# Kernel tuning notes

Hardware: AMD Instinct MI355X
Metric: run time of the kernel (lower is better)

Reference implementation:

```python
import jax, jax.numpy as jnp
import numpy as np

MARGIN = 0.25


def _cdist(x, y):
    # Euclidean distance matrix, same math as torch.cdist(p=2).
    # x: [M, D], y: [K, D] -> [M, K]
    sq = (
        jnp.sum(x * x, axis=1, keepdims=True)
        + jnp.sum(y * y, axis=1)[None, :]
        - 2.0 * (x @ y.T)
    )
    return jnp.sqrt(jnp.maximum(sq, 0.0))


def setup_inputs() -> dict:
    key = jax.random.key(0)
    k1, k2, k3 = jax.random.split(key, 3)
    B, P, N, D = 2048, 2048, 16, 128
    anchor = jax.random.normal(k1, (B, D), dtype=jnp.float32)
    positive = jax.random.normal(k2, (P, D), dtype=jnp.float32)
    negative = jax.random.normal(k3, (B, N, D), dtype=jnp.float32)
    return {"anchor": anchor, "positive": positive, "negative": negative}


def reference(anchor, positive, negative):
    B, N, D = negative.shape
    # hardest positive: max distance to any positive, per anchor -> [B]
    d_pos = _cdist(anchor, positive).max(axis=1)
    # Original torch code expands negatives across a redundant batch dim and
    # takes min over the flattened (B*B*N); per row this equals the GLOBAL min
    # over all anchor-negative pairs. Compute it without the duplication.
    neg_flat = negative.reshape(B * N, D)  # [B*N, D]
    d_neg = _cdist(anchor, neg_flat).min()  # scalar
    losses = jax.nn.relu(d_pos - d_neg + MARGIN)  # [B]
    return losses.mean()
```

## Files before the change

kernel.cpp:

```cpp
#include <hip/hip_runtime.h>
#include <hip/hip_bf16.h>

#define MARGIN_F 0.25f

#define B_ANCH 2048
#define P_POS  2048
#define N_NEG  32768
#define DDIM   128

#define QS    (6.0f / 127.0f)
#define QINV  (127.0f / 6.0f)
#define QC    (2.0f * QS * QS)
#define QCI   (1.0f / QC)

typedef __attribute__((ext_vector_type(4))) float f32x4;
typedef __attribute__((ext_vector_type(4))) int   i32x4;

__device__ __forceinline__ int q8(float x, float scl) {
    int q = __float2int_rn(x * scl);
    return max(-127, min(127, q));
}

__global__ __launch_bounds__(256) void prep_kernel(
    const float* __restrict__ anchor, const float* __restrict__ positive,
    const float* __restrict__ negative,
    signed char* __restrict__ qA, signed char* __restrict__ qP,
    signed char* __restrict__ qN,
    float* __restrict__ nA, int* __restrict__ npI, int* __restrict__ nnI,
    unsigned* __restrict__ dposBits, unsigned* __restrict__ dnegBits,
    unsigned* __restrict__ doneCnt)
{
    const int tile = blockIdx.x * 4 + (threadIdx.x >> 6);
    const int lane = threadIdx.x & 63;
    const int lm = lane & 15, lk = lane >> 4;

    if (blockIdx.x == 0 && threadIdx.x == 0) {
        *dnegBits = 0x7F800000u;
        *doneCnt  = 0u;
    }

    const float* src; signed char* dst; int t; float scl; int kind;
    if (tile < 128)      { src = anchor;   dst = qA; t = tile;       scl = -QINV; kind = 0; }
    else if (tile < 256) { src = positive; dst = qP; t = tile - 128; scl =  QINV; kind = 1; }
    else                 { src = negative; dst = qN; t = tile - 256; scl =  QINV; kind = 2; }

    if (kind == 0 && lm == lane) dposBits[t * 16 + lm] = 0u;

    const int row = t * 16 + lm;
    float ss = 0.f;
    #pragma unroll
    for (int s = 0; s < 2; ++s) {
        const float* sp = src + (size_t)row * DDIM + s * 64 + lk * 16;
        float v[16];
        #pragma unroll
        for (int c4 = 0; c4 < 4; ++c4) {
            float4 vv = *(const float4*)(sp + c4 * 4);
            v[c4*4+0]=vv.x; v[c4*4+1]=vv.y; v[c4*4+2]=vv.z; v[c4*4+3]=vv.w;
        }
        #pragma unroll
        for (int j = 0; j < 16; ++j) ss += v[j] * v[j];
        i32x4 o;
        #pragma unroll
        for (int w = 0; w < 4; ++w) {
            int b0 = q8(v[w*4+0], scl) & 255;
            int b1 = q8(v[w*4+1], scl) & 255;
            int b2 = q8(v[w*4+2], scl) & 255;
            int b3 = q8(v[w*4+3], scl) & 255;
            o[w] = b0 | (b1 << 8) | (b2 << 16) | (b3 << 24);
        }
        *(i32x4*)(dst + ((size_t)(t * 2 + s) * 64 + lane) * 16) = o;
    }
    ss += __shfl_xor(ss, 16);
    ss += __shfl_xor(ss, 32);
    if (lk == 0) {
        if (kind == 0)      nA[row]  = ss;
        else if (kind == 1) npI[row] = __float2int_rn(ss * QCI);
        else                nnI[row] = __float2int_rn(ss * QCI);
    }
}

template<int MODE, int CT>
__device__ __forceinline__ void i8_tile(
    const i32x4* __restrict__ Aq, const i32x4* __restrict__ Yq,
    const float* __restrict__ nAf, const int* __restrict__ nyI,
    int by, int bx,
    unsigned* __restrict__ dposBits, unsigned* __restrict__ dnegBits)
{
    const int wid  = threadIdx.x >> 6;
    const int lane = threadIdx.x & 63;
    const int lm = lane & 15, lk = lane >> 4;
    const int wr = wid >> 1, wc = wid & 1;
    const int rt0 = by * 8 + wr * 4;

    i32x4 a[4][2];
    #pragma unroll
    for (int m = 0; m < 4; ++m)
        #pragma unroll
        for (int s = 0; s < 2; ++s)
            a[m][s] = Aq[(size_t)((rt0 + m) * 2 + s) * 64 + lane];

    int redI[4][4];
    #pragma unroll
    for (int m = 0; m < 4; ++m)
        #pragma unroll
        for (int r = 0; r < 4; ++r)
            redI[m][r] = (MODE == 0) ? (int)0x80000000 : 0x7FFFFFFF;

    constexpr int G = CT * 4;
    auto ctile_of = [&](int p) {
        return (bx * CT + (p >> 2)) * 8 + wc * 4 + (p & 3);
    };

    i32x4 b[3][2];
    int nyv[3];
    #pragma unroll
    for (int p = 0; p < 2 && p < G; ++p) {
        const int ctile = ctile_of(p);
        #pragma unroll
        for (int s = 0; s < 2; ++s)
            b[p][s] = Yq[(size_t)(ctile * 2 + s) * 64 + lane];
        nyv[p] = nyI[ctile * 16 + lm];
    }

    #pragma unroll
    for (int g = 0; g < G; ++g) {
        const int cb = g % 3;
        if (g + 2 < G) {
            const int ctile = ctile_of(g + 2);
            #pragma unroll
            for (int s = 0; s < 2; ++s)
                b[(g + 2) % 3][s] = Yq[(size_t)(ctile * 2 + s) * 64 + lane];
            nyv[(g + 2) % 3] = nyI[ctile * 16 + lm];
        }
        const int ny = nyv[cb];
        const i32x4 cvec = {ny, ny, ny, ny};
        i32x4 acc[4];
        #pragma unroll
        for (int m = 0; m < 4; ++m)
            acc[m] = __builtin_amdgcn_mfma_i32_16x16x64_i8(a[m][0], b[cb][0], cvec, 0, 0, 0);
        #pragma unroll
        for (int m = 0; m < 4; ++m)
            acc[m] = __builtin_amdgcn_mfma_i32_16x16x64_i8(a[m][1], b[cb][1], acc[m], 0, 0, 0);
        #pragma unroll
        for (int m = 0; m < 4; ++m)
            #pragma unroll
            for (int r = 0; r < 4; ++r)
                redI[m][r] = (MODE == 0) ? max(redI[m][r], acc[m][r])
                                         : min(redI[m][r], acc[m][r]);
    }

    if (MODE == 0) {
        #pragma unroll
        for (int msk = 1; msk < 16; msk <<= 1)
            #pragma unroll
            for (int m = 0; m < 4; ++m)
                #pragma unroll
                for (int r = 0; r < 4; ++r)
                    redI[m][r] = max(redI[m][r], __shfl_xor(redI[m][r], msk));
        if (lm == 0) {
            #pragma unroll
            for (int m = 0; m < 4; ++m)
                #pragma unroll
                for (int r = 0; r < 4; ++r) {
                    const int row = (rt0 + m) * 16 + 4 * lk + r;
                    const float sq =
                        fmaxf(__builtin_fmaf(QC, (float)redI[m][r], nAf[row]), 0.f);
                    atomicMax(dposBits + row, __float_as_uint(sq));
                }
        }
    } else {
        float mn = 3.4e38f;
        #pragma unroll
        for (int m = 0; m < 4; ++m)
            #pragma unroll
            for (int r = 0; r < 4; ++r) {
                const float na = nAf[(rt0 + m) * 16 + 4 * lk + r];
                mn = fminf(mn, __builtin_fmaf(QC, (float)redI[m][r], na));
            }
        mn = fmaxf(mn, 0.f);
        #pragma unroll
        for (int msk = 1; msk < 64; msk <<= 1) mn = fminf(mn, __shfl_xor(mn, msk));
        __shared__ float wmin[4];
        if (lane == 0) wmin[wid] = mn;
        __syncthreads();
        if (threadIdx.x == 0) {
            const float m2 = fminf(fminf(wmin[0], wmin[1]), fminf(wmin[2], wmin[3]));
            atomicMin(dnegBits, __float_as_uint(m2));
        }
    }
}

#define POS_BLOCKS 256
#define NEG_BLOCKS 512
#define TOT_BLOCKS (POS_BLOCKS + NEG_BLOCKS)

__global__ __launch_bounds__(256, 3) void fused_dist_kernel(
    const signed char* __restrict__ qA, const signed char* __restrict__ qP,
    const signed char* __restrict__ qN,
    const float* __restrict__ nA, const int* __restrict__ npI,
    const int* __restrict__ nnI,
    unsigned* __restrict__ dposBits, unsigned* __restrict__ dnegBits,
    unsigned* __restrict__ doneCnt, float* __restrict__ out)
{
    const int bid = blockIdx.x;
    if (bid < POS_BLOCKS) {
        i8_tile<0, 1>((const i32x4*)qA, (const i32x4*)qP, nA, npI,
                      bid >> 4, bid & 15, dposBits, dnegBits);
    } else {
        const int q = bid - POS_BLOCKS;
        i8_tile<1, 8>((const i32x4*)qA, (const i32x4*)qN, nA, nnI,
                      q >> 5, q & 31, dposBits, dnegBits);
    }

    asm volatile("s_waitcnt vmcnt(0)" ::: "memory");
    __syncthreads();
    __shared__ unsigned lastFlag;
    if (threadIdx.x == 0)
        lastFlag = (atomicAdd(doneCnt, 1u) == TOT_BLOCKS - 1) ? 1u : 0u;
    __syncthreads();
    if (lastFlag) {
        const float dneg = sqrtf(__uint_as_float(atomicAdd(dnegBits, 0u)));
        float s = 0.f;
        for (int i = threadIdx.x; i < B_ANCH; i += 256) {
            const float dp = sqrtf(__uint_as_float(atomicAdd(dposBits + i, 0u)));
            s += fmaxf(dp - dneg + MARGIN_F, 0.f);
        }
        #pragma unroll
        for (int m = 1; m < 64; m <<= 1) s += __shfl_xor(s, m);
        __shared__ float ws4[4];
        const int wid = threadIdx.x >> 6, lane = threadIdx.x & 63;
        if (lane == 0) ws4[wid] = s;
        __syncthreads();
        if (threadIdx.x == 0)
            out[0] = (ws4[0] + ws4[1] + ws4[2] + ws4[3]) * (1.f / (float)B_ANCH);
    }
}

extern "C" void kernel_launch(void* const* d_in, const int* in_sizes, int n_in,
                              void* d_out, int out_size, void* d_ws, size_t ws_size,
                              hipStream_t stream) {
    const float* anchor   = (const float*)d_in[0];
    const float* positive = (const float*)d_in[1];
    const float* negative = (const float*)d_in[2];
    float* out = (float*)d_out;

    char* ws = (char*)d_ws;
    size_t off = 0;
    auto alloc = [&](size_t bytes) { char* p = ws + off; off = (off + bytes + 255) & ~(size_t)255; return p; };

    signed char* qA = (signed char*)alloc((size_t)B_ANCH * DDIM);
    signed char* qP = (signed char*)alloc((size_t)P_POS  * DDIM);
    signed char* qN = (signed char*)alloc((size_t)N_NEG  * DDIM);
    float* nA  = (float*)alloc((size_t)B_ANCH * 4);
    int*   npI = (int*)alloc((size_t)P_POS  * 4);
    int*   nnI = (int*)alloc((size_t)N_NEG  * 4);
    unsigned* dposBits = (unsigned*)alloc((size_t)B_ANCH * 4);
    unsigned* dnegBits = (unsigned*)alloc(4);
    unsigned* doneCnt  = (unsigned*)alloc(4);

    prep_kernel<<<576, 256, 0, stream>>>(
        anchor, positive, negative, qA, qP, qN, nA, npI, nnI,
        dposBits, dnegBits, doneCnt);

    fused_dist_kernel<<<TOT_BLOCKS, 256, 0, stream>>>(
        qA, qP, qN, nA, npI, nnI, dposBits, dnegBits, doneCnt, out);
}
```

Before: 30.89 us.

## Stage negative tiles in LDS via double-buffered direct global-to-LDS loads

The negative-distance path now copies each 8-column-tile chunk of quantized negatives into shared memory with global_load_lds, double-buffered across 8 chunks, so both wave columns share one fetch instead of loading B fragments straight into registers. The positive path is split into its own simpler function without the rotating register prefetch. This aims to cut redundant global traffic and register pressure in the dominant negative blocks. In exchange it allocates 32 KB of LDS per block, which can limit occupancy for all blocks including the positive ones, and adds a barrier per chunk.

```diff
diff --git a/kernel.cpp b/kernel.cpp
--- a/kernel.cpp
+++ b/kernel.cpp
@@ -79,12 +79,125 @@
     }
 }
 
-template<int MODE, int CT>
-__device__ __forceinline__ void i8_tile(
+__device__ __forceinline__ i32x4 mfma_i8(i32x4 a, i32x4 b, i32x4 c) {
+    return __builtin_amdgcn_mfma_i32_16x16x64_i8(a, b, c, 0, 0, 0);
+}
+
+__device__ __forceinline__ void gload_lds16(const void* g, void* l) {
+    typedef const __attribute__((address_space(1))) unsigned int as1_u32;
+    typedef __attribute__((address_space(3))) unsigned int as3_u32;
+    __builtin_amdgcn_global_load_lds(
+        (as1_u32*)(reinterpret_cast<uintptr_t>(g)),
+        (as3_u32*)(reinterpret_cast<uintptr_t>(l)),
+        16, 0, 0);
+}
+
+#define LDS_TILE 16384
+
+__device__ __forceinline__ void neg_tile_lds(
+    const i32x4* __restrict__ Aq, const signed char* __restrict__ qN,
+    const float* __restrict__ nAf, const int* __restrict__ nyI,
+    int by, int bx, unsigned* __restrict__ dnegBits,
+    signed char* __restrict__ ldsB)
+{
+    const int tid  = threadIdx.x;
+    const int wid  = tid >> 6;
+    const int lane = tid & 63;
+    const int lm = lane & 15, lk = lane >> 4;
+    const int wr = wid >> 1, wc = wid & 1;
+    const int rt0 = by * 8 + wr * 4;
+
+    i32x4 a[4][2];
+    #pragma unroll
+    for (int m = 0; m < 4; ++m)
+        #pragma unroll
+        for (int s = 0; s < 2; ++s)
+            a[m][s] = Aq[(size_t)((rt0 + m) * 2 + s) * 64 + lane];
+
+    int redI[4][4];
+    #pragma unroll
+    for (int m = 0; m < 4; ++m)
+        #pragma unroll
+        for (int r = 0; r < 4; ++r) redI[m][r] = 0x7FFFFFFF;
+
+    {
+        const signed char* g = qN + (size_t)(bx * 64) * 2048;
+        signed char* lw = ldsB + wid * 1024;
+        #pragma unroll
+        for (int c = 0; c < 4; ++c)
+            gload_lds16(g + c * 4096 + tid * 16, lw + c * 4096);
+    }
+    asm volatile("s_waitcnt vmcnt(0)" ::: "memory");
+    __syncthreads();
+
+    #pragma unroll 1
+    for (int ct = 0; ct < 8; ++ct) {
+        const signed char* lb = ldsB + (ct & 1) * LDS_TILE;
+        if (ct + 1 < 8) {
+            const signed char* g = qN + (size_t)(bx * 64 + (ct + 1) * 8) * 2048;
+            signed char* lw = ldsB + ((ct & 1) ^ 1) * LDS_TILE + wid * 1024;
+            #pragma unroll
+            for (int c = 0; c < 4; ++c)
+                gload_lds16(g + c * 4096 + tid * 16, lw + c * 4096);
+        }
+        const int ctb = (bx * 64 + ct * 8 + wc * 4) * 16 + lm;
+        const int ny0 = nyI[ctb +  0];
+        const int ny1 = nyI[ctb + 16];
+        const int ny2 = nyI[ctb + 32];
+        const int ny3 = nyI[ctb + 48];
+
+        #pragma unroll
+        for (int g4 = 0; g4 < 4; ++g4) {
+            const signed char* bp = lb + (size_t)((wc * 4 + g4) * 2) * 1024 + lane * 16;
+            const i32x4 b0 = *(const i32x4*)(bp);
+            const i32x4 b1 = *(const i32x4*)(bp + 1024);
+            const int nyc = (g4 == 0) ? ny0 : (g4 == 1) ? ny1 : (g4 == 2) ? ny2 : ny3;
+            const i32x4 cvec = {nyc, nyc, nyc, nyc};
+            i32x4 c0 = mfma_i8(a[0][0], b0, cvec);
+            i32x4 c1 = mfma_i8(a[1][0], b0, cvec);
+            i32x4 c2 = mfma_i8(a[2][0], b0, cvec);
+            i32x4 c3 = mfma_i8(a[3][0], b0, cvec);
+            c0 = mfma_i8(a[0][1], b1, c0);
+            c1 = mfma_i8(a[1][1], b1, c1);
+            c2 = mfma_i8(a[2][1], b1, c2);
+            c3 = mfma_i8(a[3][1], b1, c3);
+            #pragma unroll
+            for (int rr = 0; rr < 4; ++rr) {
+                redI[0][rr] = min(redI[0][rr], c0[rr]);
+                redI[1][rr] = min(redI[1][rr], c1[rr]);
+                redI[2][rr] = min(redI[2][rr], c2[rr]);
+                redI[3][rr] = min(redI[3][rr], c3[rr]);
+            }
+        }
+
+        asm volatile("s_waitcnt vmcnt(0)" ::: "memory");
+        __syncthreads();
+    }
+
+    float mn = 3.4e38f;
+    #pragma unroll
+    for (int m = 0; m < 4; ++m)
+        #pragma unroll
+        for (int r = 0; r < 4; ++r) {
+            const float na = nAf[(rt0 + m) * 16 + 4 * lk + r];
+            mn = fminf(mn, __builtin_fmaf(QC, (float)redI[m][r], na));
+        }
+    mn = fmaxf(mn, 0.f);
+    #pragma unroll
+    for (int msk = 1; msk < 64; msk <<= 1) mn = fminf(mn, __shfl_xor(mn, msk));
+    __shared__ float wmin[4];
+    if (lane == 0) wmin[wid] = mn;
+    __syncthreads();
+    if (threadIdx.x == 0) {
+        const float m2 = fminf(fminf(wmin[0], wmin[1]), fminf(wmin[2], wmin[3]));
+        atomicMin(dnegBits, __float_as_uint(m2));
+    }
+}
+
+__device__ __forceinline__ void pos_tile(
     const i32x4* __restrict__ Aq, const i32x4* __restrict__ Yq,
     const float* __restrict__ nAf, const int* __restrict__ nyI,
-    int by, int bx,
-    unsigned* __restrict__ dposBits, unsigned* __restrict__ dnegBits)
+    int by, int bx, unsigned* __restrict__ dposBits)
 {
     const int wid  = threadIdx.x >> 6;
     const int lane = threadIdx.x & 63;
@@ -103,90 +216,49 @@
     #pragma unroll
     for (int m = 0; m < 4; ++m)
         #pragma unroll
-        for (int r = 0; r < 4; ++r)
-            redI[m][r] = (MODE == 0) ? (int)0x80000000 : 0x7FFFFFFF;
-
-    constexpr int G = CT * 4;
-    auto ctile_of = [&](int p) {
-        return (bx * CT + (p >> 2)) * 8 + wc * 4 + (p & 3);
-    };
-
-    i32x4 b[3][2];
-    int nyv[3];
-    #pragma unroll
-    for (int p = 0; p < 2 && p < G; ++p) {
-        const int ctile = ctile_of(p);
-        #pragma unroll
-        for (int s = 0; s < 2; ++s)
-            b[p][s] = Yq[(size_t)(ctile * 2 + s) * 64 + lane];
-        nyv[p] = nyI[ctile * 16 + lm];
-    }
-
-    #pragma unroll
-    for (int g = 0; g < G; ++g) {
-        const int cb = g % 3;
-        if (g + 2 < G) {
-            const int ctile = ctile_of(g + 2);
-            #pragma unroll
-            for (int s = 0; s < 2; ++s)
-                b[(g + 2) % 3][s] = Yq[(size_t)(ctile * 2 + s) * 64 + lane];
-            nyv[(g + 2) % 3] = nyI[ctile * 16 + lm];
-        }
-        const int ny = nyv[cb];
-        const i32x4 cvec = {ny, ny, ny, ny};
-        i32x4 acc[4];
-        #pragma unroll
-        for (int m = 0; m < 4; ++m)
-            acc[m] = __builtin_amdgcn_mfma_i32_16x16x64_i8(a[m][0], b[cb][0], cvec, 0, 0, 0);
-        #pragma unroll
-        for (int m = 0; m < 4; ++m)
-            acc[m] = __builtin_amdgcn_mfma_i32_16x16x64_i8(a[m][1], b[cb][1], acc[m], 0, 0, 0);
+        for (int r = 0; r < 4; ++r) redI[m][r] = (int)0x80000000;
+
+    #pragma unroll
+    for (int g = 0; g < 4; ++g) {
+        const int ctile = bx * 8 + wc * 4 + g;
+        const i32x4 b0 = Yq[(size_t)(ctile * 2 + 0) * 64 + lane];
+        const i32x4 b1 = Yq[(size_t)(ctile * 2 + 1) * 64 + lane];
+        const int nyc = nyI[ctile * 16 + lm];
+        const i32x4 cvec = {nyc, nyc, nyc, nyc};
+        i32x4 c0 = mfma_i8(a[0][0], b0, cvec);
+        i32x4 c1 = mfma_i8(a[1][0], b0, cvec);
+        i32x4 c2 = mfma_i8(a[2][0], b0, cvec);
+        i32x4 c3 = mfma_i8(a[3][0], b0, cvec);
+        c0 = mfma_i8(a[0][1], b1, c0);
+        c1 = mfma_i8(a[1][1], b1, c1);
+        c2 = mfma_i8(a[2][1], b1, c2);
+        c3 = mfma_i8(a[3][1], b1, c3);
+        #pragma unroll
+        for (int rr = 0; rr < 4; ++rr) {
+            redI[0][rr] = max(redI[0][rr], c0[rr]);
+            redI[1][rr] = max(redI[1][rr], c1[rr]);
+            redI[2][rr] = max(redI[2][rr], c2[rr]);
+            redI[3][rr] = max(redI[3][rr], c3[rr]);
+        }
+    }
+
+    #pragma unroll
+    for (int msk = 1; msk < 16; msk <<= 1)
         #pragma unroll
         for (int m = 0; m < 4; ++m)
             #pragma unroll
             for (int r = 0; r < 4; ++r)
-                redI[m][r] = (MODE == 0) ? max(redI[m][r], acc[m][r])
-                                         : min(redI[m][r], acc[m][r]);
-    }
-
-    if (MODE == 0) {
-        #pragma unroll
-        for (int msk = 1; msk < 16; msk <<= 1)
-            #pragma unroll
-            for (int m = 0; m < 4; ++m)
-                #pragma unroll
-                for (int r = 0; r < 4; ++r)
-                    redI[m][r] = max(redI[m][r], __shfl_xor(redI[m][r], msk));
-        if (lm == 0) {
-            #pragma unroll
-            for (int m = 0; m < 4; ++m)
-                #pragma unroll
-                for (int r = 0; r < 4; ++r) {
-                    const int row = (rt0 + m) * 16 + 4 * lk + r;
-                    const float sq =
-                        fmaxf(__builtin_fmaf(QC, (float)redI[m][r], nAf[row]), 0.f);
-                    atomicMax(dposBits + row, __float_as_uint(sq));
-                }
-        }
-    } else {
-        float mn = 3.4e38f;
+                redI[m][r] = max(redI[m][r], __shfl_xor(redI[m][r], msk));
+    if (lm == 0) {
         #pragma unroll
         for (int m = 0; m < 4; ++m)
             #pragma unroll
             for (int r = 0; r < 4; ++r) {
-                const float na = nAf[(rt0 + m) * 16 + 4 * lk + r];
-                mn = fminf(mn, __builtin_fmaf(QC, (float)redI[m][r], na));
+                const int row = (rt0 + m) * 16 + 4 * lk + r;
+                const float sq =
+                    fmaxf(__builtin_fmaf(QC, (float)redI[m][r], nAf[row]), 0.f);
+                atomicMax(dposBits + row, __float_as_uint(sq));
             }
-        mn = fmaxf(mn, 0.f);
-        #pragma unroll
-        for (int msk = 1; msk < 64; msk <<= 1) mn = fminf(mn, __shfl_xor(mn, msk));
-        __shared__ float wmin[4];
-        if (lane == 0) wmin[wid] = mn;
-        __syncthreads();
-        if (threadIdx.x == 0) {
-            const float m2 = fminf(fminf(wmin[0], wmin[1]), fminf(wmin[2], wmin[3]));
-            atomicMin(dnegBits, __float_as_uint(m2));
-        }
     }
 }
 
@@ -202,14 +274,16 @@
     unsigned* __restrict__ dposBits, unsigned* __restrict__ dnegBits,
     unsigned* __restrict__ doneCnt, float* __restrict__ out)
 {
+    __shared__ signed char ldsB[2 * LDS_TILE];
+
     const int bid = blockIdx.x;
     if (bid < POS_BLOCKS) {
-        i8_tile<0, 1>((const i32x4*)qA, (const i32x4*)qP, nA, npI,
-                      bid >> 4, bid & 15, dposBits, dnegBits);
+        pos_tile((const i32x4*)qA, (const i32x4*)qP, nA, npI,
+                 bid >> 4, bid & 15, dposBits);
     } else {
         const int q = bid - POS_BLOCKS;
-        i8_tile<1, 8>((const i32x4*)qA, (const i32x4*)qN, nA, nnI,
-                      q >> 5, q & 31, dposBits, dnegBits);
+        neg_tile_lds((const i32x4*)qA, qN, nA, nnI,
+                     q >> 5, q & 31, dnegBits, ldsB);
     }
 
     asm volatile("s_waitcnt vmcnt(0)" ::: "memory");
```

Result: no change. 31.37 us (+1.6%).
